# Kernel optimization log

Measured on AMD Instinct MI355X. Metric: run time of the kernel, lower is better.

Reference implementation:

```python
import jax, jax.numpy as jnp
import numpy as np

B, M, H, E, N_ITEMS, N_USERS = 1024, 50, 128, 128, 100000, 1000


def setup_inputs() -> dict:
    key = jax.random.key(0)
    ks = jax.random.split(key, 16)
    s = 0.05
    return {
        "input_embedding": jax.random.normal(ks[0], (B, 1, E), jnp.float32),
        "hidden": jax.random.normal(ks[1], (1, B, H), jnp.float32),
        "inter_output": jax.random.normal(ks[2], (B, M, H), jnp.float32),
        "delta_t_h": jax.random.uniform(ks[3], (B,), jnp.float32),
        "user_list": jax.random.randint(ks[4], (B,), 0, N_USERS),
        # GRU params (input size 2*E since use_attn, single layer)
        "gru_w_ih": jax.random.normal(ks[5], (3 * H, 2 * E), jnp.float32) * s,
        "gru_w_hh": jax.random.normal(ks[6], (3 * H, H), jnp.float32) * s,
        "gru_b_ih": jax.random.normal(ks[7], (3 * H,), jnp.float32) * s,
        "gru_b_hh": jax.random.normal(ks[8], (3 * H,), jnp.float32) * s,
        # output projection
        "lin_W": jax.random.normal(ks[9], (N_ITEMS, H), jnp.float32) * s,
        "lin_b": jax.random.normal(ks[10], (N_ITEMS,), jnp.float32) * s,
        # per-user expert params ('cat' attention path)
        "cat_W": jax.random.normal(ks[11], (N_USERS, H, 2 * H), jnp.float32) * s,
        "cat_b": jax.random.normal(ks[12], (N_USERS, H), jnp.float32) * s,
        "scale_W": jax.random.normal(ks[13], (N_USERS, 1, H), jnp.float32) * s,
        "scale_b": jax.random.normal(ks[14], (N_USERS, 1), jnp.float32) * s,
    }


def reference(input_embedding, hidden, inter_output, delta_t_h, user_list,
              gru_w_ih, gru_w_hh, gru_b_ih, gru_b_hh,
              lin_W, lin_b, cat_W, cat_b, scale_W, scale_b):
    b, m, h = inter_output.shape
    # dropout in eval mode (p effectively 0) -> identity
    embedded_input = input_embedding
    hidden_t = jnp.transpose(hidden, (1, 0, 2))            # [B,1,H]
    # per-user 'cat' attention: gather each example's expert weights
    cat_in = jnp.concatenate(
        [jnp.broadcast_to(hidden_t, (b, m, h)), inter_output], axis=2)  # [B,M,2H]
    Wc = cat_W[user_list]                                   # [B,H,2H]
    bc = cat_b[user_list]                                   # [B,H]
    result = jnp.tanh(jnp.einsum('bmi,bhi->bmh', cat_in, Wc) + bc[:, None, :])
    Ws = scale_W[user_list]                                 # [B,1,H]
    bs = scale_b[user_list]                                 # [B,1]
    energies = jnp.einsum('bmh,boh->bmo', result, Ws) + bs[:, None, :]  # [B,M,1]
    attn_weights = jax.nn.softmax(energies[..., 0], axis=1)             # [B,M]
    context = jnp.einsum('bm,bmh->bh', attn_weights, inter_output)[:, None, :]  # [B,1,H]
    gru_in = jnp.concatenate([embedded_input, context], axis=2)         # [B,1,2E]
    # single-step GRU (PyTorch gate layout: r, z, n)
    x = gru_in[:, 0, :]
    h0 = hidden[0]                                          # [B,H]
    gi = x @ gru_w_ih.T + gru_b_ih                          # [B,3H]
    gh = h0 @ gru_w_hh.T + gru_b_hh
    i_r, i_z, i_n = jnp.split(gi, 3, axis=1)
    h_r, h_z, h_n = jnp.split(gh, 3, axis=1)
    r = jax.nn.sigmoid(i_r + h_r)
    z = jax.nn.sigmoid(i_z + h_z)
    n = jnp.tanh(i_n + r * h_n)
    h_new = (1.0 - z) * n + z * h0                          # [B,H]
    gru_output = h_new[:, None, :]                          # [B,1,H]
    output = gru_output @ lin_W.T + lin_b                   # [B,1,N_ITEMS]
    return (output, h_new[None], embedded_input, gru_output, attn_weights)
```

## Files before the change

### kernel.cpp

```cpp
#include <hip/hip_runtime.h>
#include <math.h>

#define NB 1024
#define NM 50
#define NH 128
#define NI 100000

constexpr size_t OFF_H   = (size_t)NB * NI;
constexpr size_t OFF_EMB = OFF_H   + (size_t)NB * NH;
constexpr size_t OFF_GRU = OFF_EMB + (size_t)NB * NH;
constexpr size_t OFF_ATT = OFF_GRU + (size_t)NB * NH;

typedef __attribute__((ext_vector_type(8))) short bf16x8;
typedef __attribute__((ext_vector_type(4))) float f32x4;

static __device__ __forceinline__ unsigned short f2bf(float x) {
    unsigned int u = __float_as_uint(x);
    return (unsigned short)((u + 0x7FFFu + ((u >> 16) & 1u)) >> 16);
}
static __device__ __forceinline__ float bf2f(unsigned short v) {
    return __uint_as_float((unsigned int)v << 16);
}
static __device__ __forceinline__ float fast_tanh(float x) {
    float cx = fminf(fmaxf(x, -15.0f), 15.0f);
    float e = __expf(2.0f * cx);
    return (e - 1.0f) / (e + 1.0f);
}
static __device__ __forceinline__ float fast_sigmoid(float x) {
    float cx = fminf(fmaxf(x, -30.0f), 30.0f);
    return 1.0f / (1.0f + __expf(-cx));
}
static __device__ __forceinline__ bf16x8 pack8(float4 f0, float4 f1) {
    bf16x8 p;
    p[0] = (short)f2bf(f0.x); p[1] = (short)f2bf(f0.y);
    p[2] = (short)f2bf(f0.z); p[3] = (short)f2bf(f0.w);
    p[4] = (short)f2bf(f1.x); p[5] = (short)f2bf(f1.y);
    p[6] = (short)f2bf(f1.z); p[7] = (short)f2bf(f1.w);
    return p;
}

__global__ __launch_bounds__(256) void convW_kernel(
    const float* __restrict__ W, unsigned short* __restrict__ Wbf)
{
    const int n8 = NI * NH / 8;
    for (int i = blockIdx.x * 256 + threadIdx.x; i < n8; i += gridDim.x * 256) {
        const float* s = W + (size_t)i * 8;
        bf16x8 p = pack8(*(const float4*)s, *(const float4*)(s + 4));
        __builtin_nontemporal_store(p, reinterpret_cast<bf16x8*>(Wbf + (size_t)i * 8));
    }
}

__global__ __launch_bounds__(256) void attn_mfma(
    const float* __restrict__ hidden,
    const float* __restrict__ inter,
    const int*   __restrict__ user_list,
    const float* __restrict__ cat_W,
    const float* __restrict__ cat_b,
    const float* __restrict__ scale_W,
    float* __restrict__ attn_out,
    float* __restrict__ context)
{
    const int b    = blockIdx.x;
    const int tid  = threadIdx.x;
    const int lane = tid & 63;
    const int wave = tid >> 6;

    __shared__ __align__(16) unsigned short A[64 * 256];
    __shared__ float e_sm[64];
    __shared__ float attn_sm[64];

    const int u = user_list[b];

    for (int c = tid; c < 2048; c += 256) {
        int r = c >> 5, s = c & 31;
        float4 f0, f1;
        if (s < 16) {
            const float* src = hidden + (size_t)b * NH + s * 8;
            f0 = *(const float4*)src; f1 = *(const float4*)(src + 4);
        } else if (r < NM) {
            const float* src = inter + ((size_t)b * NM + r) * NH + (s - 16) * 8;
            f0 = *(const float4*)src; f1 = *(const float4*)(src + 4);
        } else {
            f0 = (float4){0,0,0,0}; f1 = f0;
        }
        int byte = (r * 512 + s * 16) ^ ((r & 7) << 4);
        *reinterpret_cast<bf16x8*>((char*)A + byte) = pack8(f0, f1);
    }
    if (tid < 64) e_sm[tid] = 0.0f;
    __syncthreads();

    const int lrow = lane & 15;
    const int lk8  = (lane >> 4) * 8;

    float bc[2], ws[2];
    #pragma unroll
    for (int nf = 0; nf < 2; ++nf) {
        int h = wave * 32 + nf * 16 + lrow;
        bc[nf] = cat_b[(size_t)u * NH + h];
        ws[nf] = scale_W[(size_t)u * NH + h];
    }

    f32x4 acc[4][2];
    #pragma unroll
    for (int mf = 0; mf < 4; ++mf)
        #pragma unroll
        for (int nf = 0; nf < 2; ++nf)
            acc[mf][nf] = (f32x4){0,0,0,0};

    #pragma unroll
    for (int ks = 0; ks < 8; ++ks) {
        bf16x8 bfr[2];
        #pragma unroll
        for (int nf = 0; nf < 2; ++nf) {
            int h = wave * 32 + nf * 16 + lrow;
            const float* wp = cat_W + ((size_t)u * NH + h) * 256 + ks * 32 + lk8;
            bfr[nf] = pack8(*(const float4*)wp, *(const float4*)(wp + 4));
        }
        #pragma unroll
        for (int mf = 0; mf < 4; ++mf) {
            int row  = mf * 16 + lrow;
            int byte = (row * 512 + ks * 64 + lk8 * 2) ^ ((row & 7) << 4);
            bf16x8 a = *reinterpret_cast<const bf16x8*>((char*)A + byte);
            acc[mf][0] = __builtin_amdgcn_mfma_f32_16x16x32_bf16(a, bfr[0], acc[mf][0], 0, 0, 0);
            acc[mf][1] = __builtin_amdgcn_mfma_f32_16x16x32_bf16(a, bfr[1], acc[mf][1], 0, 0, 0);
        }
    }

    #pragma unroll
    for (int mf = 0; mf < 4; ++mf) {
        #pragma unroll
        for (int j = 0; j < 4; ++j) {
            float s = fast_tanh(acc[mf][0][j] + bc[0]) * ws[0]
                    + fast_tanh(acc[mf][1][j] + bc[1]) * ws[1];
            s += __shfl_xor(s, 1); s += __shfl_xor(s, 2);
            s += __shfl_xor(s, 4); s += __shfl_xor(s, 8);
            if (lrow == 0) atomicAdd(&e_sm[mf * 16 + (lane >> 4) * 4 + j], s);
        }
    }
    __syncthreads();

    if (tid < 64) {
        float x = (tid < NM) ? e_sm[tid] : -INFINITY;
        float mx = x;
        #pragma unroll
        for (int s = 1; s < 64; s <<= 1) mx = fmaxf(mx, __shfl_xor(mx, s));
        float ex = (tid < NM) ? __expf(x - mx) : 0.0f;
        float sum = ex;
        #pragma unroll
        for (int s = 1; s < 64; s <<= 1) sum += __shfl_xor(sum, s);
        float aw = ex / sum;
        attn_sm[tid] = aw;
        if (tid < NM) attn_out[(size_t)b * NM + tid] = aw;
    }
    __syncthreads();

    if (tid < NH) {
        float c = 0.0f;
        #pragma unroll
        for (int m = 0; m < NM; ++m) {
            int byte = (m * 512 + (NH + tid) * 2) ^ ((m & 7) << 4);
            c = fmaf(attn_sm[m], bf2f(*reinterpret_cast<const unsigned short*>((char*)A + byte)), c);
        }
        context[(size_t)b * NH + tid] = c;
    }
}

__global__ __launch_bounds__(128) void gru_kernel(
    const float* __restrict__ emb, const float* __restrict__ hidden,
    const float* __restrict__ context,
    const float* __restrict__ w_ih, const float* __restrict__ w_hh,
    const float* __restrict__ b_ih, const float* __restrict__ b_hh,
    float* __restrict__ out_h, float* __restrict__ out_emb, float* __restrict__ out_gru)
{
    const int b0 = blockIdx.x * 4;
    const int t  = threadIdx.x;

    __shared__ float x_sm[4][2 * NH];
    __shared__ float h_sm[4][NH];
    #pragma unroll
    for (int bb = 0; bb < 4; ++bb) {
        x_sm[bb][t]      = emb[(size_t)(b0 + bb) * NH + t];
        x_sm[bb][NH + t] = context[(size_t)(b0 + bb) * NH + t];
        h_sm[bb][t]      = hidden[(size_t)(b0 + bb) * NH + t];
    }
    __syncthreads();

    const float* wr = w_ih + (size_t)t * 256;
    const float* wz = w_ih + (size_t)(NH + t) * 256;
    const float* wn = w_ih + (size_t)(2 * NH + t) * 256;
    float gr[4], gz[4], gn[4];
    #pragma unroll
    for (int bb = 0; bb < 4; ++bb) { gr[bb] = b_ih[t]; gz[bb] = b_ih[NH + t]; gn[bb] = b_ih[2 * NH + t]; }
    for (int i4 = 0; i4 < 64; ++i4) {
        float4 wr4 = *(const float4*)(wr + i4 * 4);
        float4 wz4 = *(const float4*)(wz + i4 * 4);
        float4 wn4 = *(const float4*)(wn + i4 * 4);
        #pragma unroll
        for (int bb = 0; bb < 4; ++bb) {
            float4 x4 = *(const float4*)(&x_sm[bb][i4 * 4]);
            gr[bb] += wr4.x * x4.x + wr4.y * x4.y + wr4.z * x4.z + wr4.w * x4.w;
            gz[bb] += wz4.x * x4.x + wz4.y * x4.y + wz4.z * x4.z + wz4.w * x4.w;
            gn[bb] += wn4.x * x4.x + wn4.y * x4.y + wn4.z * x4.z + wn4.w * x4.w;
        }
    }
    const float* vr = w_hh + (size_t)t * NH;
    const float* vz = w_hh + (size_t)(NH + t) * NH;
    const float* vn = w_hh + (size_t)(2 * NH + t) * NH;
    float hr[4], hz[4], hn[4];
    #pragma unroll
    for (int bb = 0; bb < 4; ++bb) { hr[bb] = b_hh[t]; hz[bb] = b_hh[NH + t]; hn[bb] = b_hh[2 * NH + t]; }
    for (int i4 = 0; i4 < 32; ++i4) {
        float4 vr4 = *(const float4*)(vr + i4 * 4);
        float4 vz4 = *(const float4*)(vz + i4 * 4);
        float4 vn4 = *(const float4*)(vn + i4 * 4);
        #pragma unroll
        for (int bb = 0; bb < 4; ++bb) {
            float4 h4 = *(const float4*)(&h_sm[bb][i4 * 4]);
            hr[bb] += vr4.x * h4.x + vr4.y * h4.y + vr4.z * h4.z + vr4.w * h4.w;
            hz[bb] += vz4.x * h4.x + vz4.y * h4.y + vz4.z * h4.z + vz4.w * h4.w;
            hn[bb] += vn4.x * h4.x + vn4.y * h4.y + vn4.z * h4.z + vn4.w * h4.w;
        }
    }
    #pragma unroll
    for (int bb = 0; bb < 4; ++bb) {
        float r = fast_sigmoid(gr[bb] + hr[bb]);
        float z = fast_sigmoid(gz[bb] + hz[bb]);
        float n = fast_tanh(gn[bb] + r * hn[bb]);
        float h0 = h_sm[bb][t];
        float hnew = (1.0f - z) * n + z * h0;
        size_t o = (size_t)(b0 + bb) * NH + t;
        out_h[o]   = hnew;
        out_gru[o] = hnew;
        out_emb[o] = x_sm[bb][t];
    }
}

template<bool PRE>
__global__ __launch_bounds__(256, 4) void out_mfma(
    const float* __restrict__ hnew,
    const float* __restrict__ lin_W,
    const unsigned short* __restrict__ Wbf,
    const float* __restrict__ lin_b,
    float* __restrict__ out)
{
    const int L  = blockIdx.x;
    const int wg = (L & 7) * 782 + (L >> 3);
    const int mb = wg & 15;
    const int nb = wg >> 4;

    const int tid  = threadIdx.x;
    const int lane = tid & 63;
    const int wave = tid >> 6;

    const int b0 = mb * 64;
    const int n0 = nb * 256 + wave * 64;

    __shared__ __align__(16) unsigned char smem[32 * 260 * 4];
    unsigned short* As = (unsigned short*)smem;
    float (*Cs)[260]   = (float(*)[260])smem;

    for (int c = tid; c < 1024; c += 256) {
        int r = c >> 4;
        int s = c & 15;
        const float* src = hnew + (size_t)(b0 + r) * NH + s * 8;
        bf16x8 p = pack8(*(const float4*)src, *(const float4*)(src + 4));
        int byte = (r * 256 + s * 16) ^ ((r & 7) << 4);
        *reinterpret_cast<bf16x8*>((char*)As + byte) = p;
    }
    __syncthreads();

    const int lrow = lane & 15;
    const int g    = lane >> 4;
    const int lk8  = g * 8;

    f32x4 acc[4][4];
    #pragma unroll
    for (int mf = 0; mf < 4; ++mf)
        #pragma unroll
        for (int nf = 0; nf < 4; ++nf)
            acc[mf][nf] = (f32x4){0,0,0,0};

    #pragma unroll
    for (int ks = 0; ks < 4; ++ks) {
        bf16x8 av[4];
        #pragma unroll
        for (int mf = 0; mf < 4; ++mf) {
            int row  = mf * 16 + lrow;
            int byte = (row * 256 + ks * 64 + lk8 * 2) ^ ((row & 7) << 4);
            av[mf] = *reinterpret_cast<const bf16x8*>((char*)As + byte);
        }
        bf16x8 bv[4];
        #pragma unroll
        for (int nf = 0; nf < 4; ++nf) {
            int n = n0 + nf * 16 + lrow;
            const size_t nrow = (size_t)(n < NI ? n : 0) * NH;
            if (PRE) {
                bv[nf] = *reinterpret_cast<const bf16x8*>(Wbf + nrow + ks * 32 + lk8);
            } else {
                const float* wr = lin_W + nrow + ks * 32 + lk8;
                bv[nf] = pack8(*(const float4*)wr, *(const float4*)(wr + 4));
            }
        }
        #pragma unroll
        for (int nf = 0; nf < 4; ++nf)
            #pragma unroll
            for (int mf = 0; mf < 4; ++mf)
                acc[mf][nf] = __builtin_amdgcn_mfma_f32_16x16x32_bf16(
                    bv[nf], av[mf], acc[mf][nf], 0, 0, 0);
    }

    f32x4 bias4[4];
    #pragma unroll
    for (int nf = 0; nf < 4; ++nf) {
        int nq = n0 + nf * 16 + g * 4;
        if (nq > NI - 4) nq = NI - 4;
        const float4 bv = *(const float4*)(&lin_b[nq]);
        bias4[nf] = (f32x4){bv.x, bv.y, bv.z, bv.w};
    }

    #pragma unroll
    for (int half = 0; half < 2; ++half) {
        __syncthreads();
        #pragma unroll
        for (int mf2 = 0; mf2 < 2; ++mf2) {
            int mf = half * 2 + mf2;
            int rloc = mf2 * 16 + lrow;
            #pragma unroll
            for (int nf = 0; nf < 4; ++nf) {
                int colq = wave * 64 + nf * 16 + g * 4;
                *(f32x4*)(&Cs[rloc][colq]) = acc[mf][nf] + bias4[nf];
            }
        }
        __syncthreads();
        #pragma unroll
        for (int p = 0; p < 8; ++p) {
            int rloc = p * 4 + wave;
            int col4 = lane * 4;
            int n    = nb * 256 + col4;
            if (n < NI) {
                f32x4 v = *(const f32x4*)(&Cs[rloc][col4]);
                __builtin_nontemporal_store(v,
                    (f32x4*)(&out[(size_t)(b0 + half * 32 + rloc) * NI + n]));
            }
        }
    }
}

extern "C" void kernel_launch(void* const* d_in, const int* in_sizes, int n_in,
                              void* d_out, int out_size, void* d_ws, size_t ws_size,
                              hipStream_t stream) {
    const float* emb      = (const float*)d_in[0];
    const float* hidden   = (const float*)d_in[1];
    const float* inter    = (const float*)d_in[2];
    const int*   user     = (const int*)  d_in[4];
    const float* w_ih     = (const float*)d_in[5];
    const float* w_hh     = (const float*)d_in[6];
    const float* b_ih     = (const float*)d_in[7];
    const float* b_hh     = (const float*)d_in[8];
    const float* lin_W    = (const float*)d_in[9];
    const float* lin_b    = (const float*)d_in[10];
    const float* cat_W    = (const float*)d_in[11];
    const float* cat_b    = (const float*)d_in[12];
    const float* scale_W  = (const float*)d_in[13];

    float* out = (float*)d_out;
    float* ctx = (float*)d_ws;
    unsigned short* Wbf = (unsigned short*)((char*)d_ws + 512 * 1024);
    const size_t need = 512 * 1024 + (size_t)NI * NH * 2;
    const bool pre = (ws_size >= need);

    attn_mfma<<<NB, 256, 0, stream>>>(hidden, inter, user, cat_W, cat_b, scale_W,
                                      out + OFF_ATT, ctx);
    gru_kernel<<<NB / 4, 128, 0, stream>>>(emb, hidden, ctx, w_ih, w_hh, b_ih, b_hh,
                                           out + OFF_H, out + OFF_EMB, out + OFF_GRU);
    if (pre) {
        convW_kernel<<<2048, 256, 0, stream>>>(lin_W, Wbf);
        out_mfma<true><<<6256, 256, 0, stream>>>(out + OFF_H, lin_W, Wbf, lin_b, out);
    } else {
        out_mfma<false><<<6256, 256, 0, stream>>>(out + OFF_H, lin_W, nullptr, lin_b, out);
    }
}
```

Before: 207.1 us.

## Fuse attention, GRU step and weight conversion into one kernel

Merges the per-batch attention kernel, the GRU kernel and the lin_W bf16 conversion into a single launch with one block per batch row. The context vector now stays in shared memory instead of going through workspace, and three launches become one. In exchange, each GRU block handles one batch row instead of four, so the GRU weights are re-read four times as often. The conversion work is also spread across the attention blocks, which may lengthen that kernel.

```diff
diff --git a/kernel.cpp b/kernel.cpp
--- a/kernel.cpp
+++ b/kernel.cpp
@@ -39,26 +39,25 @@
     return p;
 }
 
-__global__ __launch_bounds__(256) void convW_kernel(
-    const float* __restrict__ W, unsigned short* __restrict__ Wbf)
-{
-    const int n8 = NI * NH / 8;
-    for (int i = blockIdx.x * 256 + threadIdx.x; i < n8; i += gridDim.x * 256) {
-        const float* s = W + (size_t)i * 8;
-        bf16x8 p = pack8(*(const float4*)s, *(const float4*)(s + 4));
-        __builtin_nontemporal_store(p, reinterpret_cast<bf16x8*>(Wbf + (size_t)i * 8));
-    }
-}
-
-__global__ __launch_bounds__(256) void attn_mfma(
+template<bool PRE>
+__global__ __launch_bounds__(256) void fused_kernel(
+    const float* __restrict__ emb,
     const float* __restrict__ hidden,
     const float* __restrict__ inter,
     const int*   __restrict__ user_list,
     const float* __restrict__ cat_W,
     const float* __restrict__ cat_b,
     const float* __restrict__ scale_W,
+    const float* __restrict__ w_ih,
+    const float* __restrict__ w_hh,
+    const float* __restrict__ b_ih,
+    const float* __restrict__ b_hh,
+    const float* __restrict__ lin_W,
+    unsigned short* __restrict__ Wbf,
     float* __restrict__ attn_out,
-    float* __restrict__ context)
+    float* __restrict__ out_h,
+    float* __restrict__ out_emb,
+    float* __restrict__ out_gru)
 {
     const int b    = blockIdx.x;
     const int tid  = threadIdx.x;
@@ -68,6 +67,16 @@
     __shared__ __align__(16) unsigned short A[64 * 256];
     __shared__ float e_sm[64];
     __shared__ float attn_sm[64];
+    __shared__ float x_sm[2 * NH];
+
+    if (PRE) {
+        const int n8 = NI * NH / 8;
+        for (int i = b * 256 + tid; i < n8; i += NB * 256) {
+            const float* s = lin_W + (size_t)i * 8;
+            bf16x8 p = pack8(*(const float4*)s, *(const float4*)(s + 4));
+            __builtin_nontemporal_store(p, reinterpret_cast<bf16x8*>(Wbf + (size_t)i * 8));
+        }
+    }
 
     const int u = user_list[b];
 
@@ -161,77 +170,49 @@
             int byte = (m * 512 + (NH + tid) * 2) ^ ((m & 7) << 4);
             c = fmaf(attn_sm[m], bf2f(*reinterpret_cast<const unsigned short*>((char*)A + byte)), c);
         }
-        context[(size_t)b * NH + tid] = c;
-    }
-}
-
-__global__ __launch_bounds__(128) void gru_kernel(
-    const float* __restrict__ emb, const float* __restrict__ hidden,
-    const float* __restrict__ context,
-    const float* __restrict__ w_ih, const float* __restrict__ w_hh,
-    const float* __restrict__ b_ih, const float* __restrict__ b_hh,
-    float* __restrict__ out_h, float* __restrict__ out_emb, float* __restrict__ out_gru)
-{
-    const int b0 = blockIdx.x * 4;
-    const int t  = threadIdx.x;
-
-    __shared__ float x_sm[4][2 * NH];
-    __shared__ float h_sm[4][NH];
-    #pragma unroll
-    for (int bb = 0; bb < 4; ++bb) {
-        x_sm[bb][t]      = emb[(size_t)(b0 + bb) * NH + t];
-        x_sm[bb][NH + t] = context[(size_t)(b0 + bb) * NH + t];
-        h_sm[bb][t]      = hidden[(size_t)(b0 + bb) * NH + t];
-    }
-    __syncthreads();
-
-    const float* wr = w_ih + (size_t)t * 256;
-    const float* wz = w_ih + (size_t)(NH + t) * 256;
-    const float* wn = w_ih + (size_t)(2 * NH + t) * 256;
-    float gr[4], gz[4], gn[4];
-    #pragma unroll
-    for (int bb = 0; bb < 4; ++bb) { gr[bb] = b_ih[t]; gz[bb] = b_ih[NH + t]; gn[bb] = b_ih[2 * NH + t]; }
-    for (int i4 = 0; i4 < 64; ++i4) {
-        float4 wr4 = *(const float4*)(wr + i4 * 4);
-        float4 wz4 = *(const float4*)(wz + i4 * 4);
-        float4 wn4 = *(const float4*)(wn + i4 * 4);
-        #pragma unroll
-        for (int bb = 0; bb < 4; ++bb) {
-            float4 x4 = *(const float4*)(&x_sm[bb][i4 * 4]);
-            gr[bb] += wr4.x * x4.x + wr4.y * x4.y + wr4.z * x4.z + wr4.w * x4.w;
-            gz[bb] += wz4.x * x4.x + wz4.y * x4.y + wz4.z * x4.z + wz4.w * x4.w;
-            gn[bb] += wn4.x * x4.x + wn4.y * x4.y + wn4.z * x4.z + wn4.w * x4.w;
-        }
-    }
-    const float* vr = w_hh + (size_t)t * NH;
-    const float* vz = w_hh + (size_t)(NH + t) * NH;
-    const float* vn = w_hh + (size_t)(2 * NH + t) * NH;
-    float hr[4], hz[4], hn[4];
-    #pragma unroll
-    for (int bb = 0; bb < 4; ++bb) { hr[bb] = b_hh[t]; hz[bb] = b_hh[NH + t]; hn[bb] = b_hh[2 * NH + t]; }
-    for (int i4 = 0; i4 < 32; ++i4) {
-        float4 vr4 = *(const float4*)(vr + i4 * 4);
-        float4 vz4 = *(const float4*)(vz + i4 * 4);
-        float4 vn4 = *(const float4*)(vn + i4 * 4);
-        #pragma unroll
-        for (int bb = 0; bb < 4; ++bb) {
-            float4 h4 = *(const float4*)(&h_sm[bb][i4 * 4]);
-            hr[bb] += vr4.x * h4.x + vr4.y * h4.y + vr4.z * h4.z + vr4.w * h4.w;
-            hz[bb] += vz4.x * h4.x + vz4.y * h4.y + vz4.z * h4.z + vz4.w * h4.w;
-            hn[bb] += vn4.x * h4.x + vn4.y * h4.y + vn4.z * h4.z + vn4.w * h4.w;
-        }
-    }
-    #pragma unroll
-    for (int bb = 0; bb < 4; ++bb) {
-        float r = fast_sigmoid(gr[bb] + hr[bb]);
-        float z = fast_sigmoid(gz[bb] + hz[bb]);
-        float n = fast_tanh(gn[bb] + r * hn[bb]);
-        float h0 = h_sm[bb][t];
+        x_sm[NH + tid] = c;
+        x_sm[tid]      = emb[(size_t)b * NH + tid];
+    }
+    __syncthreads();
+
+    if (tid < NH) {
+        const int t = tid;
+        const float* wr = w_ih + (size_t)t * 256;
+        const float* wz = w_ih + (size_t)(NH + t) * 256;
+        const float* wn = w_ih + (size_t)(2 * NH + t) * 256;
+        float gr = b_ih[t], gz = b_ih[NH + t], gn = b_ih[2 * NH + t];
+        for (int i4 = 0; i4 < 64; ++i4) {
+            float4 wr4 = *(const float4*)(wr + i4 * 4);
+            float4 wz4 = *(const float4*)(wz + i4 * 4);
+            float4 wn4 = *(const float4*)(wn + i4 * 4);
+            float4 x4  = *(const float4*)(&x_sm[i4 * 4]);
+            gr += wr4.x * x4.x + wr4.y * x4.y + wr4.z * x4.z + wr4.w * x4.w;
+            gz += wz4.x * x4.x + wz4.y * x4.y + wz4.z * x4.z + wz4.w * x4.w;
+            gn += wn4.x * x4.x + wn4.y * x4.y + wn4.z * x4.z + wn4.w * x4.w;
+        }
+        const float* vr = w_hh + (size_t)t * NH;
+        const float* vz = w_hh + (size_t)(NH + t) * NH;
+        const float* vn = w_hh + (size_t)(2 * NH + t) * NH;
+        float hr = b_hh[t], hz = b_hh[NH + t], hn = b_hh[2 * NH + t];
+        const float* hvec = hidden + (size_t)b * NH;
+        for (int i4 = 0; i4 < 32; ++i4) {
+            float4 vr4 = *(const float4*)(vr + i4 * 4);
+            float4 vz4 = *(const float4*)(vz + i4 * 4);
+            float4 vn4 = *(const float4*)(vn + i4 * 4);
+            float4 h4  = *(const float4*)(hvec + i4 * 4);
+            hr += vr4.x * h4.x + vr4.y * h4.y + vr4.z * h4.z + vr4.w * h4.w;
+            hz += vz4.x * h4.x + vz4.y * h4.y + vz4.z * h4.z + vz4.w * h4.w;
+            hn += vn4.x * h4.x + vn4.y * h4.y + vn4.z * h4.z + vn4.w * h4.w;
+        }
+        float r = fast_sigmoid(gr + hr);
+        float z = fast_sigmoid(gz + hz);
+        float n = fast_tanh(gn + r * hn);
+        float h0 = hvec[t];
         float hnew = (1.0f - z) * n + z * h0;
-        size_t o = (size_t)(b0 + bb) * NH + t;
+        size_t o = (size_t)b * NH + t;
         out_h[o]   = hnew;
         out_gru[o] = hnew;
-        out_emb[o] = x_sm[bb][t];
+        out_emb[o] = x_sm[t];
     }
 }
 
@@ -364,19 +345,21 @@
     const float* scale_W  = (const float*)d_in[13];
 
     float* out = (float*)d_out;
-    float* ctx = (float*)d_ws;
-    unsigned short* Wbf = (unsigned short*)((char*)d_ws + 512 * 1024);
-    const size_t need = 512 * 1024 + (size_t)NI * NH * 2;
+    unsigned short* Wbf = (unsigned short*)d_ws;
+    const size_t need = (size_t)NI * NH * 2;
     const bool pre = (ws_size >= need);
 
-    attn_mfma<<<NB, 256, 0, stream>>>(hidden, inter, user, cat_W, cat_b, scale_W,
-                                      out + OFF_ATT, ctx);
-    gru_kernel<<<NB / 4, 128, 0, stream>>>(emb, hidden, ctx, w_ih, w_hh, b_ih, b_hh,
-                                           out + OFF_H, out + OFF_EMB, out + OFF_GRU);
     if (pre) {
-        convW_kernel<<<2048, 256, 0, stream>>>(lin_W, Wbf);
+        fused_kernel<true><<<NB, 256, 0, stream>>>(
+            emb, hidden, inter, user, cat_W, cat_b, scale_W,
+            w_ih, w_hh, b_ih, b_hh, lin_W, Wbf,
+            out + OFF_ATT, out + OFF_H, out + OFF_EMB, out + OFF_GRU);
         out_mfma<true><<<6256, 256, 0, stream>>>(out + OFF_H, lin_W, Wbf, lin_b, out);
     } else {
+        fused_kernel<false><<<NB, 256, 0, stream>>>(
+            emb, hidden, inter, user, cat_W, cat_b, scale_W,
+            w_ih, w_hh, b_ih, b_hh, lin_W, nullptr,
+            out + OFF_ATT, out + OFF_H, out + OFF_EMB, out + OFF_GRU);
         out_mfma<false><<<6256, 256, 0, stream>>>(out + OFF_H, lin_W, nullptr, lin_b, out);
     }
 }
```

Measured after the change: 244.5 us. 18.1% more time.
